# Kernel tuning notes

Measured on AMD Instinct MI355X. Metric: run time of the kernel, lower is better.

## Reference

```python
import jax, jax.numpy as jnp
import numpy as np

BATCH = 4
N_MELS, T_LEN, PATCH = 128, 512, 16
D_MODEL, D_INNER, D_STATE, DT_RANK, D_CONV = 512, 1024, 16, 32, 4
DEPTH, N_CLASSES = 4, 10


def _silu(x):
    return x * jax.nn.sigmoid(x)


def _ln(x, w, b):
    m = x.mean(-1, keepdims=True)
    v = ((x - m) ** 2).mean(-1, keepdims=True)
    return (x - m) * jax.lax.rsqrt(v + 1e-5) * w + b


def _causal_conv(x, w, b):
    # x: (B, L, D); w: (D, K) depthwise causal conv (mamba conv1d)
    K, L = w.shape[-1], x.shape[1]
    xp = jnp.pad(x, ((0, 0), (K - 1, 0), (0, 0)))
    y = sum(xp[:, k:k + L, :] * w[:, k] for k in range(K))
    return y + b


def _ssm(xc, conv_w, conv_b, xproj_w, dtproj_w, dtproj_b, A_log, Dp):
    # One directional selective scan (mamba S6).
    u = _silu(_causal_conv(xc, conv_w, conv_b))              # (B,L,Di)
    xdbl = jnp.einsum('bld,ed->ble', u, xproj_w)             # (B,L,dt_rank+2S)
    dtr, Bm, Cm = jnp.split(xdbl, [DT_RANK, DT_RANK + D_STATE], axis=-1)
    dt = jax.nn.softplus(jnp.einsum('blr,dr->bld', dtr, dtproj_w) + dtproj_b)
    A = -jnp.exp(A_log)                                      # (Di,S)
    dA = jnp.exp(dt[..., None] * A)                          # (B,L,Di,S)
    dBu = (dt * u)[..., None] * Bm[:, :, None, :]            # (B,L,Di,S)

    def comb(e1, e2):
        a1, b1 = e1
        a2, b2 = e2
        return a1 * a2, a2 * b1 + b2

    _, h = jax.lax.associative_scan(comb, (dA, dBu), axis=1)  # parallel linear recurrence
    return jnp.einsum('blds,bls->bld', h, Cm) + u * Dp


def _forward(x, patch_w, patch_b, in_proj_w, conv_w_f, conv_b_f, conv_w_b, conv_b_b,
             xproj_w_f, xproj_w_b, dtproj_w_f, dtproj_b_f, dtproj_w_b, dtproj_b_b,
             A_log_f, A_log_b, D_f, D_b, out_proj_w, norm_w, norm_b,
             normf_w, normf_b, ln_w, ln_b, fc1_w, fc1_b, fc2_w, fc2_b):
    B = x.shape[0]
    # Patch embed: conv with kernel == stride -> reshape + einsum
    xp = x.reshape(B, 1, N_MELS // PATCH, PATCH, T_LEN // PATCH, PATCH)
    tok = jnp.einsum('bchpwq,dcpq->bhwd', xp, patch_w) + patch_b
    h = tok.reshape(B, -1, D_MODEL)                           # (B, 256, D)
    for i in range(DEPTH):
        xn = _ln(h, norm_w[i], norm_b[i])
        xz = jnp.einsum('bld,ed->ble', xn, in_proj_w[i])
        xc, z = jnp.split(xz, 2, axis=-1)
        y_f = _ssm(xc, conv_w_f[i], conv_b_f[i], xproj_w_f[i],
                   dtproj_w_f[i], dtproj_b_f[i], A_log_f[i], D_f[i])
        y_b = jnp.flip(_ssm(jnp.flip(xc, 1), conv_w_b[i], conv_b_b[i], xproj_w_b[i],
                            dtproj_w_b[i], dtproj_b_b[i], A_log_b[i], D_b[i]), 1)
        y = (y_f + y_b) * _silu(z)                            # bimamba v2: fwd + flipped bwd, gated
        h = h + jnp.einsum('bld,ed->ble', y, out_proj_w[i])
    h = _ln(h, normf_w, normf_b)
    feat = h.mean(axis=1)                                     # pooled features (B, D)
    c = _ln(feat, ln_w, ln_b)
    c = jnp.maximum(c @ fc1_w.T + fc1_b, 0.0)
    return c @ fc2_w.T + fc2_b


def setup_inputs() -> dict:
    ks = iter(jax.random.split(jax.random.key(0), 64))

    def rn(shape, s=0.02):
        return jax.random.normal(next(ks), shape, jnp.float32) * s

    inp = {}
    inp['x'] = jax.random.normal(next(ks), (BATCH, 1, N_MELS, T_LEN), jnp.float32)
    inp['patch_w'] = rn((D_MODEL, 1, PATCH, PATCH))
    inp['patch_b'] = jnp.zeros((D_MODEL,), jnp.float32)
    inp['in_proj_w'] = rn((DEPTH, 2 * D_INNER, D_MODEL))
    A_init = jnp.log(jnp.tile(jnp.arange(1, D_STATE + 1, dtype=jnp.float32), (DEPTH, D_INNER, 1)))
    for sfx in ('f', 'b'):
        inp[f'conv_w_{sfx}'] = rn((DEPTH, D_INNER, D_CONV), 0.2)
        inp[f'conv_b_{sfx}'] = jnp.zeros((DEPTH, D_INNER), jnp.float32)
        inp[f'xproj_w_{sfx}'] = rn((DEPTH, DT_RANK + 2 * D_STATE, D_INNER))
        inp[f'dtproj_w_{sfx}'] = rn((DEPTH, D_INNER, DT_RANK), 0.1)
        inp[f'dtproj_b_{sfx}'] = jnp.full((DEPTH, D_INNER), -4.6, jnp.float32)  # softplus -> dt ~ 0.01
        inp[f'A_log_{sfx}'] = A_init
        inp[f'D_{sfx}'] = jnp.ones((DEPTH, D_INNER), jnp.float32)
    inp['out_proj_w'] = rn((DEPTH, D_MODEL, D_INNER))
    inp['norm_w'] = jnp.ones((DEPTH, D_MODEL), jnp.float32)
    inp['norm_b'] = jnp.zeros((DEPTH, D_MODEL), jnp.float32)
    inp['normf_w'] = jnp.ones((D_MODEL,), jnp.float32)
    inp['normf_b'] = jnp.zeros((D_MODEL,), jnp.float32)
    inp['ln_w'] = jnp.ones((D_MODEL,), jnp.float32)
    inp['ln_b'] = jnp.zeros((D_MODEL,), jnp.float32)
    inp['fc1_w'] = rn((512, D_MODEL))
    inp['fc1_b'] = jnp.zeros((512,), jnp.float32)
    inp['fc2_w'] = rn((N_CLASSES, 512))
    inp['fc2_b'] = jnp.zeros((N_CLASSES,), jnp.float32)
    return inp


def reference(x, patch_w, patch_b, in_proj_w, conv_w_f, conv_b_f, conv_w_b, conv_b_b,
              xproj_w_f, xproj_w_b, dtproj_w_f, dtproj_b_f, dtproj_w_b, dtproj_b_b,
              A_log_f, A_log_b, D_f, D_b, out_proj_w, norm_w, norm_b,
              normf_w, normf_b, ln_w, ln_b, fc1_w, fc1_b, fc2_w, fc2_b):
    return _forward(x, patch_w, patch_b, in_proj_w, conv_w_f, conv_b_f, conv_w_b, conv_b_b,
                    xproj_w_f, xproj_w_b, dtproj_w_f, dtproj_b_f, dtproj_w_b, dtproj_b_b,
                    A_log_f, A_log_b, D_f, D_b, out_proj_w, norm_w, norm_b,
                    normf_w, normf_b, ln_w, ln_b, fc1_w, fc1_b, fc2_w, fc2_b)
```

## Files before the change

kernel.cpp:

```cpp
#include <hip/hip_runtime.h>


#define BB 4
#define LL 256
#define DM 512
#define DI 1024
#define LDST 40

typedef unsigned short u16;
typedef unsigned int u32;
typedef __attribute__((ext_vector_type(8))) short s8v;
typedef __attribute__((ext_vector_type(4))) float f4v;

__device__ __forceinline__ float silu_f(float x){ return x/(1.f+__expf(-x)); }
__device__ __forceinline__ float b2f(u16 u){
  union { u32 i; float f; } v; v.i = ((u32)u) << 16; return v.f;
}
__device__ __forceinline__ void b2x2(u32 w, float& lo, float& hi){
  union { u32 i; float f; } a, b;
  a.i = w << 16; b.i = w & 0xffff0000u;
  lo = a.f; hi = b.f;
}
__device__ __forceinline__ u16 f2bf(float f){
  union { float f; u32 u; } v; v.f = f;
  u32 r = (v.u + 0x7fffu + ((v.u >> 16) & 1u)) >> 16;
  return (u16)r;
}
__device__ __forceinline__ void split8(const float* f, s8v& hi, s8v& lo){
#pragma unroll
  for (int j = 0; j < 8; ++j){
    u16 h = f2bf(f[j]);
    float hf = b2f(h);
    hi[j] = (short)h;
    lo[j] = (short)f2bf(f[j] - hf);
  }
}

__device__ __forceinline__ float row_sum16(float p){
  union { float f; int i; } v, r;
  v.f = p;
  r.i = __builtin_amdgcn_update_dpp(0, v.i, 0x111, 0xF, 0xF, true); v.f += r.f;
  r.i = __builtin_amdgcn_update_dpp(0, v.i, 0x112, 0xF, 0xF, true); v.f += r.f;
  r.i = __builtin_amdgcn_update_dpp(0, v.i, 0x114, 0xF, 0xF, true); v.f += r.f;
  r.i = __builtin_amdgcn_update_dpp(0, v.i, 0x118, 0xF, 0xF, true); v.f += r.f;
  return v.f;
}

__device__ __forceinline__ void block_reduce2(float& a, float& b, float* sc, int nw){
  int lane = threadIdx.x & 63, wid = threadIdx.x >> 6;
#pragma unroll
  for (int o = 32; o > 0; o >>= 1){
    a += __shfl_down(a, o, 64);
    b += __shfl_down(b, o, 64);
  }
  if (lane == 0){ sc[wid*2] = a; sc[wid*2+1] = b; }
  __syncthreads();
  float ta = 0.f, tb = 0.f;
  for (int i = 0; i < nw; ++i){ ta += sc[i*2]; tb += sc[i*2+1]; }
  a = ta; b = tb;
}

__global__ __launch_bounds__(256) void convert_w_all(const float* __restrict__ inW,
    const float* __restrict__ outW, const float* __restrict__ xwF,
    const float* __restrict__ xwB, const float* __restrict__ dtwF,
    const float* __restrict__ dtwB, u16* __restrict__ inHi, u16* __restrict__ inLo,
    u16* __restrict__ outHi, u16* __restrict__ outLo, u16* __restrict__ xwHi,
    u16* __restrict__ xwLo, u16* __restrict__ dtwHi, u16* __restrict__ dtwLo){
  int lay = blockIdx.y;
  int idx = blockIdx.x*256 + threadIdx.x;
  const float4* src; ushort4* dh; ushort4* dl;
  if (idx < 262144){
    src = (const float4*)(inW + (size_t)lay*1048576) + idx;
    dh = (ushort4*)(inHi + (size_t)lay*1048576) + idx;
    dl = (ushort4*)(inLo + (size_t)lay*1048576) + idx;
  } else if (idx < 393216){
    int j = idx - 262144;
    src = (const float4*)(outW + (size_t)lay*524288) + j;
    dh = (ushort4*)(outHi + (size_t)lay*524288) + j;
    dl = (ushort4*)(outLo + (size_t)lay*524288) + j;
  } else if (idx < 409600){
    int j = idx - 393216;
    src = (const float4*)(xwF + (size_t)lay*65536) + j;
    dh = (ushort4*)(xwHi + (size_t)lay*131072) + j;
    dl = (ushort4*)(xwLo + (size_t)lay*131072) + j;
  } else if (idx < 425984){
    int j = idx - 409600;
    src = (const float4*)(xwB + (size_t)lay*65536) + j;
    dh = (ushort4*)(xwHi + (size_t)lay*131072 + 65536) + j;
    dl = (ushort4*)(xwLo + (size_t)lay*131072 + 65536) + j;
  } else if (idx < 434176){
    int j = idx - 425984;
    src = (const float4*)(dtwF + (size_t)lay*32768) + j;
    dh = (ushort4*)(dtwHi + (size_t)lay*65536) + j;
    dl = (ushort4*)(dtwLo + (size_t)lay*65536) + j;
  } else {
    int j = idx - 434176;
    src = (const float4*)(dtwB + (size_t)lay*32768) + j;
    dh = (ushort4*)(dtwHi + (size_t)lay*65536 + 32768) + j;
    dl = (ushort4*)(dtwLo + (size_t)lay*65536 + 32768) + j;
  }
  float4 v = *src;
  ushort4 h, l;
  h.x = f2bf(v.x); l.x = f2bf(v.x - b2f(h.x));
  h.y = f2bf(v.y); l.y = f2bf(v.y - b2f(h.y));
  h.z = f2bf(v.z); l.z = f2bf(v.z - b2f(h.z));
  h.w = f2bf(v.w); l.w = f2bf(v.w - b2f(h.w));
  *dh = h; *dl = l;
}

__global__ __launch_bounds__(256) void patch_embed(const float* __restrict__ x,
    const float* __restrict__ pw, const float* __restrict__ pb, float* __restrict__ h){
  __shared__ float xs[8*256];
  int blk = blockIdx.x;
  int b = blk >> 6, ph = (blk >> 3) & 7, pg = (blk >> 1) & 3, dh = blk & 1;
  int t = threadIdx.x;
  for (int idx = t; idx < 2048; idx += 256){
    int j = idx >> 8, pix = idx & 255, p = pix >> 4, q = pix & 15;
    xs[idx] = x[(size_t)(b*128 + ph*16 + p)*512 + pg*128 + j*16 + q];
  }
  __syncthreads();
  int d = dh*256 + t;
  float acc[8] = {};
  const float* wr = pw + (size_t)d*256;
  for (int i = 0; i < 256; i += 8){
    float4 w0 = *(const float4*)(wr + i);
    float4 w1 = *(const float4*)(wr + i + 4);
    float wf[8] = {w0.x,w0.y,w0.z,w0.w,w1.x,w1.y,w1.z,w1.w};
#pragma unroll
    for (int j = 0; j < 8; ++j){
#pragma unroll
      for (int jj = 0; jj < 8; ++jj)
        acc[j] = fmaf(xs[j*256 + i + jj], wf[jj], acc[j]);
    }
  }
  float bias = pb[d];
#pragma unroll
  for (int j = 0; j < 8; ++j)
    h[(size_t)(b*256 + ph*32 + pg*8 + j)*512 + d] = acc[j] + bias;
}

__global__ __launch_bounds__(256) void prep_ln(const float* __restrict__ x,
    const float* __restrict__ w, const float* __restrict__ bias, int wOff,
    u16* __restrict__ hiO, u16* __restrict__ loO, float* __restrict__ xdblZ){
  __shared__ float sc[8];
  int row = blockIdx.x, t = threadIdx.x;
  if (t < 128) xdblZ[(size_t)row*128 + t] = 0.f;
  const float* xr = x + (size_t)row*DM;
  float v0 = xr[t], v1 = xr[t + 256];
  float s = v0 + v1, ss = v0*v0 + v1*v1;
  block_reduce2(s, ss, sc, 4);
  float mean = s * (1.f/512.f);
  float var = ss * (1.f/512.f) - mean*mean;
  float inv = rsqrtf(var + 1e-5f);
  float o0 = (v0 - mean)*inv*w[wOff + t]       + bias[wOff + t];
  float o1 = (v1 - mean)*inv*w[wOff + t + 256] + bias[wOff + t + 256];
  u16 h0 = f2bf(o0), h1 = f2bf(o1);
  hiO[(size_t)row*DM + t]       = h0;
  hiO[(size_t)row*DM + t + 256] = h1;
  loO[(size_t)row*DM + t]       = f2bf(o0 - b2f(h0));
  loO[(size_t)row*DM + t + 256] = f2bf(o1 - b2f(h1));
}

__global__ __launch_bounds__(256) void prep_gate(const float* __restrict__ ybuf,
    const float* __restrict__ xz, u16* __restrict__ gHi, u16* __restrict__ gLo){
  int row = blockIdx.x, t = threadIdx.x;
  int c = t*4;
  float4 yf = *(const float4*)(ybuf + (size_t)row*DI + c);
  float4 yb = *(const float4*)(ybuf + 1048576 + (size_t)row*DI + c);
  float4 zv = *(const float4*)(xz + (size_t)row*2048 + 1024 + c);
  float g0 = (yf.x + yb.x)*silu_f(zv.x);
  float g1 = (yf.y + yb.y)*silu_f(zv.y);
  float g2 = (yf.z + yb.z)*silu_f(zv.z);
  float g3 = (yf.w + yb.w)*silu_f(zv.w);
  ushort4 h, l;
  h.x = f2bf(g0); l.x = f2bf(g0 - b2f(h.x));
  h.y = f2bf(g1); l.y = f2bf(g1 - b2f(h.y));
  h.z = f2bf(g2); l.z = f2bf(g2 - b2f(h.z));
  h.w = f2bf(g3); l.w = f2bf(g3 - b2f(h.w));
  *(ushort4*)(gHi + (size_t)row*DI + c) = h;
  *(ushort4*)(gLo + (size_t)row*DI + c) = l;
}

__global__ __launch_bounds__(256) void gemm_bf16(const u16* __restrict__ Ahi_g,
    const u16* __restrict__ Alo_g, int As, const u16* __restrict__ Bhi_g,
    const u16* __restrict__ Blo_g, int Bs, float* __restrict__ C, int Cs,
    int K, int addFlag){
  __shared__ __align__(16) u16 Ah[64*LDST], Al[64*LDST], Bh[64*LDST], Bl[64*LDST];
  int bm = blockIdx.y*64, bn = blockIdx.x*64;
  int t = threadIdx.x;
  int sr = t >> 2, sc8 = (t & 3)*8;
  int lane = t & 63, wv = t >> 6, ml = lane & 15, quad = lane >> 4;
  int mq = wv >> 1, nq = wv & 1;
  f4v acc[2][2] = {};
  for (int k0 = 0; k0 < K; k0 += 32){
    *(uint4*)&Ah[sr*LDST + sc8] = *(const uint4*)(Ahi_g + (size_t)(bm + sr)*As + k0 + sc8);
    *(uint4*)&Al[sr*LDST + sc8] = *(const uint4*)(Alo_g + (size_t)(bm + sr)*As + k0 + sc8);
    *(uint4*)&Bh[sr*LDST + sc8] = *(const uint4*)(Bhi_g + (size_t)(bn + sr)*Bs + k0 + sc8);
    *(uint4*)&Bl[sr*LDST + sc8] = *(const uint4*)(Blo_g + (size_t)(bn + sr)*Bs + k0 + sc8);
    __syncthreads();
    s8v ah[2], al2[2], bh2[2], bl2[2];
#pragma unroll
    for (int mt = 0; mt < 2; ++mt){
      int row = mq*32 + mt*16 + ml;
      ah[mt]  = *(s8v*)&Ah[row*LDST + quad*8];
      al2[mt] = *(s8v*)&Al[row*LDST + quad*8];
    }
#pragma unroll
    for (int nt = 0; nt < 2; ++nt){
      int col = nq*32 + nt*16 + ml;
      bh2[nt] = *(s8v*)&Bh[col*LDST + quad*8];
      bl2[nt] = *(s8v*)&Bl[col*LDST + quad*8];
    }
#pragma unroll
    for (int mt = 0; mt < 2; ++mt)
#pragma unroll
      for (int nt = 0; nt < 2; ++nt){
        acc[mt][nt] = __builtin_amdgcn_mfma_f32_16x16x32_bf16(ah[mt],  bh2[nt], acc[mt][nt], 0, 0, 0);
        acc[mt][nt] = __builtin_amdgcn_mfma_f32_16x16x32_bf16(al2[mt], bh2[nt], acc[mt][nt], 0, 0, 0);
        acc[mt][nt] = __builtin_amdgcn_mfma_f32_16x16x32_bf16(ah[mt],  bl2[nt], acc[mt][nt], 0, 0, 0);
      }
    __syncthreads();
  }
#pragma unroll
  for (int mt = 0; mt < 2; ++mt)
#pragma unroll
    for (int nt = 0; nt < 2; ++nt)
#pragma unroll
      for (int r = 0; r < 4; ++r){
        float* cp = C + (size_t)(bm + mq*32 + mt*16 + quad*4 + r)*Cs +
                    bn + nq*32 + nt*16 + ml;
        if (addFlag) *cp += acc[mt][nt][r];
        else         *cp  = acc[mt][nt][r];
      }
}

__global__ __launch_bounds__(256) void conv_silu_split(const float* __restrict__ xz,
    const float* __restrict__ cwF, const float* __restrict__ cbF,
    const float* __restrict__ cwB, const float* __restrict__ cbB,
    int cwOff, int cbOff, u16* __restrict__ uHi, u16* __restrict__ uLo){
  int blk = blockIdx.x;
  int dir = blk >> 8, rem = blk & 255, b = rem >> 6, lg = rem & 63;
  int l0 = lg*4;
  const float* cw = dir ? cwB : cwF;
  const float* cb = dir ? cbB : cbF;
  int t = threadIdx.x;
  int rbase = (dir*BB + b)*LL;
  for (int dd = 0; dd < 4; ++dd){
    int d = t + dd*256;
    float4 w4 = *(const float4*)(cw + cwOff + d*4);
    float wf[4] = {w4.x, w4.y, w4.z, w4.w};
    float bias = cb[cbOff + d];
#pragma unroll
    for (int r = 0; r < 4; ++r){
      int l = l0 + r;
      float acc = bias;
#pragma unroll
      for (int k = 0; k < 4; ++k){
        int li = l + k - 3;
        if (li >= 0){
          int sl = dir ? (LL-1-li) : li;
          acc = fmaf(xz[(size_t)(b*LL + sl)*2048 + d], wf[k], acc);
        }
      }
      float uval = silu_f(acc);
      u16 h = f2bf(uval);
      uHi[(size_t)(rbase + l)*DI + d] = h;
      uLo[(size_t)(rbase + l)*DI + d] = f2bf(uval - b2f(h));
    }
  }
}

__global__ __launch_bounds__(256) void gemm_xproj_splitk(const u16* __restrict__ uHi,
    const u16* __restrict__ uLo, const u16* __restrict__ xwHi,
    const u16* __restrict__ xwLo, float* __restrict__ xdbl){
  __shared__ __align__(16) u16 Ah[64*LDST], Al[64*LDST], Bh[64*LDST], Bl[64*LDST];
  int bm = blockIdx.y*64;
  int kc = blockIdx.x;
  int dir = bm >> 10;
  const u16* BhG = xwHi + dir*65536;
  const u16* BlG = xwLo + dir*65536;
  int t = threadIdx.x;
  int sr = t >> 2, sc8 = (t & 3)*8;
  int lane = t & 63, wv = t >> 6, ml = lane & 15, quad = lane >> 4;
  int mq = wv >> 1, nq = wv & 1;
  f4v acc[2][2] = {};
  for (int k0 = kc*256; k0 < kc*256 + 256; k0 += 32){
    *(uint4*)&Ah[sr*LDST + sc8] = *(const uint4*)(uHi + (size_t)(bm + sr)*1024 + k0 + sc8);
    *(uint4*)&Al[sr*LDST + sc8] = *(const uint4*)(uLo + (size_t)(bm + sr)*1024 + k0 + sc8);
    *(uint4*)&Bh[sr*LDST + sc8] = *(const uint4*)(BhG + (size_t)sr*1024 + k0 + sc8);
    *(uint4*)&Bl[sr*LDST + sc8] = *(const uint4*)(BlG + (size_t)sr*1024 + k0 + sc8);
    __syncthreads();
    s8v ah[2], al2[2], bh2[2], bl2[2];
#pragma unroll
    for (int mt = 0; mt < 2; ++mt){
      int row = mq*32 + mt*16 + ml;
      ah[mt]  = *(s8v*)&Ah[row*LDST + quad*8];
      al2[mt] = *(s8v*)&Al[row*LDST + quad*8];
    }
#pragma unroll
    for (int nt = 0; nt < 2; ++nt){
      int col = nq*32 + nt*16 + ml;
      bh2[nt] = *(s8v*)&Bh[col*LDST + quad*8];
      bl2[nt] = *(s8v*)&Bl[col*LDST + quad*8];
    }
#pragma unroll
    for (int mt = 0; mt < 2; ++mt)
#pragma unroll
      for (int nt = 0; nt < 2; ++nt){
        acc[mt][nt] = __builtin_amdgcn_mfma_f32_16x16x32_bf16(ah[mt],  bh2[nt], acc[mt][nt], 0, 0, 0);
        acc[mt][nt] = __builtin_amdgcn_mfma_f32_16x16x32_bf16(al2[mt], bh2[nt], acc[mt][nt], 0, 0, 0);
        acc[mt][nt] = __builtin_amdgcn_mfma_f32_16x16x32_bf16(ah[mt],  bl2[nt], acc[mt][nt], 0, 0, 0);
      }
    __syncthreads();
  }
#pragma unroll
  for (int mt = 0; mt < 2; ++mt)
#pragma unroll
    for (int nt = 0; nt < 2; ++nt)
#pragma unroll
      for (int r = 0; r < 4; ++r)
        atomicAdd(xdbl + (size_t)(bm + mq*32 + mt*16 + quad*4 + r)*64 +
                  nq*32 + nt*16 + ml, acc[mt][nt][r]);
}

__global__ __launch_bounds__(256) void scan_coal(
    const u16* __restrict__ uHi, const u16* __restrict__ uLo,
    const float* __restrict__ xd,
    const float* __restrict__ dtwF, const float* __restrict__ dtwB,
    const float* __restrict__ dtbF, const float* __restrict__ dtbB,
    const float* __restrict__ AlogF, const float* __restrict__ AlogB,
    const float* __restrict__ DF, const float* __restrict__ DB,
    int dtwOff, int bOff, int aOff, int dOff, float* __restrict__ y){
  __shared__ __align__(16) float dtuT[16][516];
  __shared__ __align__(16) float BCT[16][516];
  __shared__ __align__(16) float ytile[128][16];
  int blk = blockIdx.x;
  int dir = blk >> 8, b = (blk >> 6) & 3, dg = blk & 63;
  int t = threadIdx.x;
  int rbase = (dir*BB + b)*LL;
  const float* Alog = dir ? AlogB : AlogF;
  const float* Dpt  = dir ? DB : DF;
  {
    int d_local = t & 15, lc = t >> 4;
    int d = dg*16 + d_local;
    const float* dtw = (dir ? dtwB : dtwF) + dtwOff + (size_t)d*32;
    float wreg[32];
#pragma unroll
    for (int k = 0; k < 32; k += 4){
      float4 w4 = *(const float4*)(dtw + k);
      wreg[k] = w4.x; wreg[k+1] = w4.y; wreg[k+2] = w4.z; wreg[k+3] = w4.w;
    }
    float bias = (dir ? dtbB : dtbF)[bOff + d];
    for (int i = 0; i < 16; ++i){
      int l = lc*16 + i;
      const float* xr = xd + (size_t)(rbase + l)*64;
      float acc = bias;
#pragma unroll
      for (int k = 0; k < 32; k += 4){
        float4 v = *(const float4*)(xr + k);
        acc = fmaf(v.x, wreg[k],   acc);
        acc = fmaf(v.y, wreg[k+1], acc);
        acc = fmaf(v.z, wreg[k+2], acc);
        acc = fmaf(v.w, wreg[k+3], acc);
      }
      float dtv = (acc > 15.f) ? acc : log1pf(__expf(acc));
      size_t ub = (size_t)(rbase + l)*DI + d;
      float uval = b2f(uHi[ub]) + b2f(uLo[ub]);
      float2 pr = {dtv, uval};
      *(float2*)&dtuT[d_local][l*2] = pr;
    }
  }
  {
    int h8 = t & 7, lb = t >> 3;
    for (int pass = 0; pass < 8; ++pass){
      int l = pass*32 + lb;
      float4 v = *(const float4*)(xd + (size_t)(rbase + l)*64 + 32 + h8*4);
      if (h8 < 4){
        int s0 = h8*4;
        BCT[s0+0][l*2] = v.x; BCT[s0+1][l*2] = v.y;
        BCT[s0+2][l*2] = v.z; BCT[s0+3][l*2] = v.w;
      } else {
        int s0 = (h8-4)*4;
        BCT[s0+0][l*2+1] = v.x; BCT[s0+1][l*2+1] = v.y;
        BCT[s0+2][l*2+1] = v.z; BCT[s0+3][l*2+1] = v.w;
      }
    }
  }
  int s = t & 15, dl = t >> 4;
  float Av = -__expf(Alog[aOff + dg*256 + t]);
  float Dp = Dpt[dOff + dg*16 + dl];
  __syncthreads();
  float h = 0.f;
  for (int half = 0; half < 2; ++half){
    for (int l0 = half*128; l0 < half*128 + 128; l0 += 4){
      float4 du01 = *(const float4*)&dtuT[dl][l0*2];
      float4 du23 = *(const float4*)&dtuT[dl][l0*2 + 4];
      float4 bc01 = *(const float4*)&BCT[s][l0*2];
      float4 bc23 = *(const float4*)&BCT[s][l0*2 + 4];
      float dtv[4] = {du01.x, du01.z, du23.x, du23.z};
      float uv[4]  = {du01.y, du01.w, du23.y, du23.w};
      float Bv[4]  = {bc01.x, bc01.z, bc23.x, bc23.z};
      float Cv[4]  = {bc01.y, bc01.w, bc23.y, bc23.w};
#pragma unroll
      for (int i = 0; i < 4; ++i){
        float a = __expf(dtv[i] * Av);
        h = fmaf(a, h, dtv[i]*uv[i]*Bv[i]);
        float p = h * Cv[i];
        float sum = row_sum16(p);
        if (s == 15){
          int lr = (l0 + i) & 127;
          ytile[lr][dl] = fmaf(uv[i], Dp, sum);
        }
      }
    }
    __syncthreads();
    {
      int d4 = t & 3, lh = t >> 2;
      for (int pass = 0; pass < 2; ++pass){
        int lr = pass*64 + lh;
        int l = half*128 + lr;
        int lo = dir ? (255 - l) : l;
        float4 vv = *(const float4*)&ytile[lr][d4*4];
        *(float4*)(y + (size_t)(rbase + lo)*DI + dg*16 + d4*4) = vv;
      }
    }
    __syncthreads();
  }
}

__global__ __launch_bounds__(256) void ln_kernel(const float* __restrict__ x,
    const float* __restrict__ w, const float* __restrict__ bias,
    float* __restrict__ y){
  __shared__ float sc[8];
  int row = blockIdx.x, t = threadIdx.x;
  const float* xr = x + (size_t)row*DM;
  float v0 = xr[t], v1 = xr[t + 256];
  float s = v0 + v1, ss = v0*v0 + v1*v1;
  block_reduce2(s, ss, sc, 4);
  float mean = s * (1.f/512.f);
  float var = ss * (1.f/512.f) - mean*mean;
  float inv = rsqrtf(var + 1e-5f);
  float* yr = y + (size_t)row*DM;
  yr[t]       = (v0 - mean)*inv*w[t]       + bias[t];
  yr[t + 256] = (v1 - mean)*inv*w[t + 256] + bias[t + 256];
}

__global__ __launch_bounds__(256) void pool_kernel(const float* __restrict__ hn,
    float* __restrict__ feat){
  __shared__ float part[4][64];
  int b = blockIdx.x >> 3, dg = blockIdx.x & 7;
  int t = threadIdx.x, dl = t & 63, lq = t >> 6;
  const float* p = hn + (size_t)(b*256 + lq*64)*512 + dg*64 + dl;
  float s = 0.f;
#pragma unroll 4
  for (int i = 0; i < 64; ++i) s += p[(size_t)i*512];
  part[lq][dl] = s;
  __syncthreads();
  if (t < 64)
    feat[b*512 + dg*64 + t] =
        (part[0][t] + part[1][t] + part[2][t] + part[3][t]) * (1.f/256.f);
}

__global__ __launch_bounds__(512) void head_kernel(const float* __restrict__ feat,
    const float* __restrict__ lnw, const float* __restrict__ lnb,
    const float* __restrict__ fc1w, const float* __restrict__ fc1b,
    const float* __restrict__ fc2w, const float* __restrict__ fc2b,
    float* __restrict__ out){
  __shared__ float sc[16];
  __shared__ float cbuf[512];
  __shared__ float rbuf[512];
  int b = blockIdx.x, t = threadIdx.x;
  float v = feat[b*512 + t];
  float s = v, ss = v*v;
  block_reduce2(s, ss, sc, 8);
  float mean = s * (1.f/512.f);
  float var = ss * (1.f/512.f) - mean*mean;
  float inv = rsqrtf(var + 1e-5f);
  cbuf[t] = (v - mean)*inv*lnw[t] + lnb[t];
  __syncthreads();
  float a = fc1b[t];
  const float* w1 = fc1w + (size_t)t*512;
  for (int i = 0; i < 512; i += 8){
    float4 w0 = *(const float4*)(w1 + i);
    float4 w4 = *(const float4*)(w1 + i + 4);
    float wf[8] = {w0.x,w0.y,w0.z,w0.w,w4.x,w4.y,w4.z,w4.w};
#pragma unroll
    for (int j = 0; j < 8; ++j) a = fmaf(cbuf[i + j], wf[j], a);
  }
  rbuf[t] = fmaxf(a, 0.f);
  __syncthreads();
  if (t < 10){
    float a2 = fc2b[t];
    const float* w2 = fc2w + (size_t)t*512;
    for (int i = 0; i < 512; ++i) a2 = fmaf(rbuf[i], w2[i], a2);
    out[b*10 + t] = a2;
  }
}

extern "C" void kernel_launch(void* const* d_in, const int* in_sizes, int n_in,
                              void* d_out, int out_size, void* d_ws, size_t ws_size,
                              hipStream_t stream) {
  (void)in_sizes; (void)n_in; (void)out_size; (void)ws_size;
  const float* x          = (const float*)d_in[0];
  const float* patch_w    = (const float*)d_in[1];
  const float* patch_b    = (const float*)d_in[2];
  const float* in_proj_w  = (const float*)d_in[3];
  const float* conv_w_f   = (const float*)d_in[4];
  const float* conv_b_f   = (const float*)d_in[5];
  const float* xproj_w_f  = (const float*)d_in[6];
  const float* dtproj_w_f = (const float*)d_in[7];
  const float* dtproj_b_f = (const float*)d_in[8];
  const float* A_log_f    = (const float*)d_in[9];
  const float* D_f        = (const float*)d_in[10];
  const float* conv_w_b   = (const float*)d_in[11];
  const float* conv_b_b   = (const float*)d_in[12];
  const float* xproj_w_b  = (const float*)d_in[13];
  const float* dtproj_w_b = (const float*)d_in[14];
  const float* dtproj_b_b = (const float*)d_in[15];
  const float* A_log_b    = (const float*)d_in[16];
  const float* D_b        = (const float*)d_in[17];
  const float* out_proj_w = (const float*)d_in[18];
  const float* norm_w     = (const float*)d_in[19];
  const float* norm_b     = (const float*)d_in[20];
  const float* normf_w    = (const float*)d_in[21];
  const float* normf_b    = (const float*)d_in[22];
  const float* ln_w       = (const float*)d_in[23];
  const float* ln_b       = (const float*)d_in[24];
  const float* fc1_w      = (const float*)d_in[25];
  const float* fc1_b      = (const float*)d_in[26];
  const float* fc2_w      = (const float*)d_in[27];
  const float* fc2_b      = (const float*)d_in[28];

  float* ws   = (float*)d_ws;
  float* hbuf = ws;
  float* xz   = ws + 524288;
  u16*   uHi  = (u16*)(ws + 2621440);
  u16*   uLo  = (u16*)(ws + 3670016);
  float* xdbl = ws + 4718592;
  float* ybuf = ws + 6946816;
  float* hn   = ws + 9043968;
  float* feat = ws + 11141120;
  u16*   xnHi = (u16*)hn;
  u16*   xnLo = (u16*)(ws + 9306112);
  u16*   gHi  = (u16*)(ws + 2621440);
  u16*   gLo  = (u16*)(ws + 3145728);
  u16*   inHi4 = (u16*)(ws + 11145216);
  u16*   inLo4 = (u16*)(ws + 13242368);
  u16*   outHi4= (u16*)(ws + 15339520);
  u16*   outLo4= (u16*)(ws + 16388096);
  u16*   xwHi4 = (u16*)(ws + 17436672);
  u16*   xwLo4 = (u16*)(ws + 17698816);
  u16*   dtwHi4= (u16*)(ws + 17960960);
  u16*   dtwLo4= (u16*)(ws + 18092032);

  convert_w_all<<<dim3(1728, 4), 256, 0, stream>>>(
      in_proj_w, out_proj_w, xproj_w_f, xproj_w_b, dtproj_w_f, dtproj_w_b,
      inHi4, inLo4, outHi4, outLo4, xwHi4, xwLo4, dtwHi4, dtwLo4);
  patch_embed<<<256, 256, 0, stream>>>(x, patch_w, patch_b, hbuf);
  for (int i = 0; i < 4; ++i){
    prep_ln<<<1024, 256, 0, stream>>>(hbuf, norm_w, norm_b, i*512, xnHi, xnLo, xdbl);
    gemm_bf16<<<dim3(32, 16), 256, 0, stream>>>(
        xnHi, xnLo, 512, inHi4 + (size_t)i*1048576, inLo4 + (size_t)i*1048576,
        512, xz, 2048, 512, 0);
    conv_silu_split<<<512, 256, 0, stream>>>(
        xz, conv_w_f, conv_b_f, conv_w_b, conv_b_b, i*4096, i*1024, uHi, uLo);
    gemm_xproj_splitk<<<dim3(4, 32), 256, 0, stream>>>(
        uHi, uLo, xwHi4 + (size_t)i*131072, xwLo4 + (size_t)i*131072, xdbl);
    scan_coal<<<512, 256, 0, stream>>>(
        uHi, uLo, xdbl, dtproj_w_f, dtproj_w_b, dtproj_b_f, dtproj_b_b,
        A_log_f, A_log_b, D_f, D_b, i*32768, i*1024, i*16384, i*1024, ybuf);
    prep_gate<<<1024, 256, 0, stream>>>(ybuf, xz, gHi, gLo);
    gemm_bf16<<<dim3(8, 16), 256, 0, stream>>>(
        gHi, gLo, 1024, outHi4 + (size_t)i*524288, outLo4 + (size_t)i*524288,
        1024, hbuf, 512, 1024, 1);
  }
  ln_kernel<<<1024, 256, 0, stream>>>(hbuf, normf_w, normf_b, hn);
  pool_kernel<<<32, 256, 0, stream>>>(hn, feat);
  head_kernel<<<4, 512, 0, stream>>>(feat, ln_w, ln_b, fc1_w, fc1_b, fc2_w, fc2_b,
                                     (float*)d_out);
}
```

Baseline: 624.9 us.

## Split scan state dimension across blocks and sum partial outputs in gate

```diff
diff --git a/kernel.cpp b/kernel.cpp
--- a/kernel.cpp
+++ b/kernel.cpp
@@ -16,11 +16,6 @@
 __device__ __forceinline__ float b2f(u16 u){
   union { u32 i; float f; } v; v.i = ((u32)u) << 16; return v.f;
 }
-__device__ __forceinline__ void b2x2(u32 w, float& lo, float& hi){
-  union { u32 i; float f; } a, b;
-  a.i = w << 16; b.i = w & 0xffff0000u;
-  lo = a.f; hi = b.f;
-}
 __device__ __forceinline__ u16 f2bf(float f){
   union { float f; u32 u; } v; v.f = f;
   u32 r = (v.u + 0x7fffu + ((v.u >> 16) & 1u)) >> 16;
@@ -36,13 +31,12 @@
   }
 }
 
-__device__ __forceinline__ float row_sum16(float p){
+__device__ __forceinline__ float row_sum8(float p){
   union { float f; int i; } v, r;
   v.f = p;
   r.i = __builtin_amdgcn_update_dpp(0, v.i, 0x111, 0xF, 0xF, true); v.f += r.f;
   r.i = __builtin_amdgcn_update_dpp(0, v.i, 0x112, 0xF, 0xF, true); v.f += r.f;
   r.i = __builtin_amdgcn_update_dpp(0, v.i, 0x114, 0xF, 0xF, true); v.f += r.f;
-  r.i = __builtin_amdgcn_update_dpp(0, v.i, 0x118, 0xF, 0xF, true); v.f += r.f;
   return v.f;
 }
 
@@ -161,17 +155,20 @@
   loO[(size_t)row*DM + t + 256] = f2bf(o1 - b2f(h1));
 }
 
-__global__ __launch_bounds__(256) void prep_gate(const float* __restrict__ ybuf,
-    const float* __restrict__ xz, u16* __restrict__ gHi, u16* __restrict__ gLo){
+__global__ __launch_bounds__(256) void prep_gate(const float* __restrict__ ypA,
+    const float* __restrict__ ypB, const float* __restrict__ xz,
+    u16* __restrict__ gHi, u16* __restrict__ gLo){
   int row = blockIdx.x, t = threadIdx.x;
   int c = t*4;
-  float4 yf = *(const float4*)(ybuf + (size_t)row*DI + c);
-  float4 yb = *(const float4*)(ybuf + 1048576 + (size_t)row*DI + c);
+  float4 a0 = *(const float4*)(ypA + (size_t)row*DI + c);
+  float4 b0 = *(const float4*)(ypB + (size_t)row*DI + c);
+  float4 a1 = *(const float4*)(ypA + 1048576 + (size_t)row*DI + c);
+  float4 b1 = *(const float4*)(ypB + 1048576 + (size_t)row*DI + c);
   float4 zv = *(const float4*)(xz + (size_t)row*2048 + 1024 + c);
-  float g0 = (yf.x + yb.x)*silu_f(zv.x);
-  float g1 = (yf.y + yb.y)*silu_f(zv.y);
-  float g2 = (yf.z + yb.z)*silu_f(zv.z);
-  float g3 = (yf.w + yb.w)*silu_f(zv.w);
+  float g0 = ((a0.x + b0.x) + (a1.x + b1.x))*silu_f(zv.x);
+  float g1 = ((a0.y + b0.y) + (a1.y + b1.y))*silu_f(zv.y);
+  float g2 = ((a0.z + b0.z) + (a1.z + b1.z))*silu_f(zv.z);
+  float g3 = ((a0.w + b0.w) + (a1.w + b1.w))*silu_f(zv.w);
   ushort4 h, l;
   h.x = f2bf(g0); l.x = f2bf(g0 - b2f(h.x));
   h.y = f2bf(g1); l.y = f2bf(g1 - b2f(h.y));
@@ -323,38 +320,47 @@
                   nq*32 + nt*16 + ml, acc[mt][nt][r]);
 }
 
-__global__ __launch_bounds__(256) void scan_coal(
+__global__ __launch_bounds__(256) void scan_split(
     const u16* __restrict__ uHi, const u16* __restrict__ uLo,
     const float* __restrict__ xd,
     const float* __restrict__ dtwF, const float* __restrict__ dtwB,
     const float* __restrict__ dtbF, const float* __restrict__ dtbB,
     const float* __restrict__ AlogF, const float* __restrict__ AlogB,
     const float* __restrict__ DF, const float* __restrict__ DB,
-    int dtwOff, int bOff, int aOff, int dOff, float* __restrict__ y){
-  __shared__ __align__(16) float dtuT[16][516];
-  __shared__ __align__(16) float BCT[16][516];
-  __shared__ __align__(16) float ytile[128][16];
+    int dtwOff, int bOff, int aOff, int dOff,
+    float* __restrict__ ypA, float* __restrict__ ypB){
+  __shared__ __align__(16) float dtuT[32][260];
+  __shared__ __align__(16) float BCT[8][260];
+  __shared__ __align__(16) float ytile[128][32];
   int blk = blockIdx.x;
-  int dir = blk >> 8, b = (blk >> 6) & 3, dg = blk & 63;
+  int dg = blk & 31, b = (blk >> 5) & 3, dir = (blk >> 7) & 1, sh = blk >> 8;
   int t = threadIdx.x;
   int rbase = (dir*BB + b)*LL;
   const float* Alog = dir ? AlogB : AlogF;
   const float* Dpt  = dir ? DB : DF;
+  float* yp = sh ? ypB : ypA;
+  int d_l = t & 31, lc = t >> 5;
+  int dstage = dg*32 + d_l;
+  float wreg[32];
   {
-    int d_local = t & 15, lc = t >> 4;
-    int d = dg*16 + d_local;
-    const float* dtw = (dir ? dtwB : dtwF) + dtwOff + (size_t)d*32;
-    float wreg[32];
+    const float* dtw = (dir ? dtwB : dtwF) + dtwOff + (size_t)dstage*32;
 #pragma unroll
     for (int k = 0; k < 32; k += 4){
       float4 w4 = *(const float4*)(dtw + k);
       wreg[k] = w4.x; wreg[k+1] = w4.y; wreg[k+2] = w4.z; wreg[k+3] = w4.w;
     }
-    float bias = (dir ? dtbB : dtbF)[bOff + d];
+  }
+  float dbias = (dir ? dtbB : dtbF)[bOff + dstage];
+  int s = t & 7, dl = t >> 3;
+  float Av = -__expf(Alog[aOff + (dg*32 + dl)*16 + sh*8 + s]);
+  float Dp = Dpt[dOff + dg*32 + dl];
+  float h = 0.f;
+  for (int half = 0; half < 2; ++half){
     for (int i = 0; i < 16; ++i){
-      int l = lc*16 + i;
+      int ll = lc*16 + i;
+      int l = half*128 + ll;
       const float* xr = xd + (size_t)(rbase + l)*64;
-      float acc = bias;
+      float acc = dbias;
 #pragma unroll
       for (int k = 0; k < 32; k += 4){
         float4 v = *(const float4*)(xr + k);
@@ -364,35 +370,28 @@
         acc = fmaf(v.w, wreg[k+3], acc);
       }
       float dtv = (acc > 15.f) ? acc : log1pf(__expf(acc));
-      size_t ub = (size_t)(rbase + l)*DI + d;
+      size_t ub = (size_t)(rbase + l)*DI + dstage;
       float uval = b2f(uHi[ub]) + b2f(uLo[ub]);
       float2 pr = {dtv, uval};
-      *(float2*)&dtuT[d_local][l*2] = pr;
-    }
-  }
-  {
-    int h8 = t & 7, lb = t >> 3;
-    for (int pass = 0; pass < 8; ++pass){
-      int l = pass*32 + lb;
-      float4 v = *(const float4*)(xd + (size_t)(rbase + l)*64 + 32 + h8*4);
-      if (h8 < 4){
-        int s0 = h8*4;
-        BCT[s0+0][l*2] = v.x; BCT[s0+1][l*2] = v.y;
-        BCT[s0+2][l*2] = v.z; BCT[s0+3][l*2] = v.w;
-      } else {
-        int s0 = (h8-4)*4;
-        BCT[s0+0][l*2+1] = v.x; BCT[s0+1][l*2+1] = v.y;
-        BCT[s0+2][l*2+1] = v.z; BCT[s0+3][l*2+1] = v.w;
-      }
-    }
-  }
-  int s = t & 15, dl = t >> 4;
-  float Av = -__expf(Alog[aOff + dg*256 + t]);
-  float Dp = Dpt[dOff + dg*16 + dl];
-  __syncthreads();
-  float h = 0.f;
-  for (int half = 0; half < 2; ++half){
-    for (int l0 = half*128; l0 < half*128 + 128; l0 += 4){
+      *(float2*)&dtuT[d_l][ll*2] = pr;
+    }
+    {
+      int q = t & 3, lb = t >> 2;
+      for (int pass = 0; pass < 2; ++pass){
+        int ll = pass*64 + lb;
+        int l = half*128 + ll;
+        int col = (q < 2) ? (32 + sh*8 + q*4) : (48 + sh*8 + (q - 2)*4);
+        float4 v = *(const float4*)(xd + (size_t)(rbase + l)*64 + col);
+        int parity = (q < 2) ? 0 : 1;
+        int s0 = (q & 1)*4;
+        BCT[s0+0][ll*2 + parity] = v.x;
+        BCT[s0+1][ll*2 + parity] = v.y;
+        BCT[s0+2][ll*2 + parity] = v.z;
+        BCT[s0+3][ll*2 + parity] = v.w;
+      }
+    }
+    __syncthreads();
+    for (int l0 = 0; l0 < 128; l0 += 4){
       float4 du01 = *(const float4*)&dtuT[dl][l0*2];
       float4 du23 = *(const float4*)&dtuT[dl][l0*2 + 4];
       float4 bc01 = *(const float4*)&BCT[s][l0*2];
@@ -405,23 +404,23 @@
       for (int i = 0; i < 4; ++i){
         float a = __expf(dtv[i] * Av);
         h = fmaf(a, h, dtv[i]*uv[i]*Bv[i]);
-        float p = h * Cv[i];
-        float sum = row_sum16(p);
-        if (s == 15){
-          int lr = (l0 + i) & 127;
-          ytile[lr][dl] = fmaf(uv[i], Dp, sum);
+        float sum = row_sum8(h * Cv[i]);
+        if (s == 7){
+          float o = sum;
+          if (sh == 0) o = fmaf(uv[i], Dp, o);
+          ytile[l0 + i][dl] = o;
         }
       }
     }
     __syncthreads();
     {
-      int d4 = t & 3, lh = t >> 2;
-      for (int pass = 0; pass < 2; ++pass){
-        int lr = pass*64 + lh;
+      int d8 = t & 7, lh = t >> 3;
+      for (int pass = 0; pass < 4; ++pass){
+        int lr = pass*32 + lh;
         int l = half*128 + lr;
         int lo = dir ? (255 - l) : l;
-        float4 vv = *(const float4*)&ytile[lr][d4*4];
-        *(float4*)(y + (size_t)(rbase + lo)*DI + dg*16 + d4*4) = vv;
+        float4 vv = *(const float4*)&ytile[lr][d8*4];
+        *(float4*)(yp + (size_t)(rbase + lo)*DI + dg*32 + d8*4) = vv;
       }
     }
     __syncthreads();
@@ -537,7 +536,8 @@
   u16*   uHi  = (u16*)(ws + 2621440);
   u16*   uLo  = (u16*)(ws + 3670016);
   float* xdbl = ws + 4718592;
-  float* ybuf = ws + 6946816;
+  float* ypB  = ws + 4849664;
+  float* ypA  = ws + 6946816;
   float* hn   = ws + 9043968;
   float* feat = ws + 11141120;
   u16*   xnHi = (u16*)hn;
@@ -566,10 +566,10 @@
         xz, conv_w_f, conv_b_f, conv_w_b, conv_b_b, i*4096, i*1024, uHi, uLo);
     gemm_xproj_splitk<<<dim3(4, 32), 256, 0, stream>>>(
         uHi, uLo, xwHi4 + (size_t)i*131072, xwLo4 + (size_t)i*131072, xdbl);
-    scan_coal<<<512, 256, 0, stream>>>(
+    scan_split<<<512, 256, 0, stream>>>(
         uHi, uLo, xdbl, dtproj_w_f, dtproj_w_b, dtproj_b_f, dtproj_b_b,
-        A_log_f, A_log_b, D_f, D_b, i*32768, i*1024, i*16384, i*1024, ybuf);
-    prep_gate<<<1024, 256, 0, stream>>>(ybuf, xz, gHi, gLo);
+        A_log_f, A_log_b, D_f, D_b, i*32768, i*1024, i*16384, i*1024, ypA, ypB);
+    prep_gate<<<1024, 256, 0, stream>>>(ypA, ypB, xz, gHi, gLo);
     gemm_bf16<<<dim3(8, 16), 256, 0, stream>>>(
         gHi, gLo, 1024, outHi4 + (size_t)i*524288, outLo4 + (size_t)i*524288,
         1024, hbuf, 512, 1024, 1);
```

Measured after the change: 642.6 us. 2.8% more time.
